# Performance work log

Measured on AMD Instinct MI355X. Metric: run time of the kernel, lower is better.

## Reference

```python
import jax, jax.numpy as jnp
import numpy as np

C_LOGIT = 10.0  # logit range hyperparameter (use_tanh=True)


def setup_inputs() -> dict:
    key = jax.random.key(0)
    ks = jax.random.split(key, 7)
    B, S, D = 64, 2048, 512
    s = 1.0 / np.sqrt(D)
    return {
        "query": jax.random.normal(ks[0], (B, D), jnp.float32),
        "ref": jax.random.normal(ks[1], (B, S, D), jnp.float32),
        "Wq_w": jax.random.uniform(ks[2], (D, D), jnp.float32, -s, s),
        "Wq_b": jax.random.uniform(ks[3], (D,), jnp.float32, -s, s),
        "Wr_w": jax.random.uniform(ks[4], (D, D), jnp.float32, -s, s),  # Conv1d k=1 == Linear
        "Wr_b": jax.random.uniform(ks[5], (D,), jnp.float32, -s, s),
        "value": jax.random.uniform(ks[6], (D,), jnp.float32, -s, s),
    }


def reference(query, ref, Wq_w, Wq_b, Wr_w, Wr_b, value):
    # query: [B, D], ref: [B, S, D]
    q = query @ Wq_w.T + Wq_b                                  # [B, D]  (Wq linear)
    r = jnp.einsum("bsd,ed->bse", ref, Wr_w) + Wr_b            # [B, S, D] (Conv1d k=1 over permuted ref)
    h = jnp.tanh(q[:, None, :] + r)                            # broadcast query over seq_len
    logits = jnp.einsum("bsd,d->bs", h, value)                 # <v, tanh(Wq q + Wr r)>
    logits = C_LOGIT * jnp.tanh(logits)                        # use_tanh=True
    ref_out = jnp.transpose(r, (0, 2, 1))                      # [B, D, S] as returned by torch branch
    return ref_out, logits
```

## Files before the change

### kernel.cpp

```cpp
#include <hip/hip_runtime.h>
#include <stdint.h>

#define NB  64
#define SEQ 2048
#define DIM 512
#define NS  (NB*SEQ)

typedef __bf16 bf16x8 __attribute__((ext_vector_type(8)));
typedef float  f32x4  __attribute__((ext_vector_type(4)));
typedef unsigned int u32;
typedef unsigned short u16;
typedef unsigned int u32x4 __attribute__((ext_vector_type(4)));

__device__ __forceinline__ u32 pk_bf16(float a, float b){
  union {float f; u32 i;} x, y; x.f = a; y.f = b;
  return ((x.i + 0x8000u) >> 16) | ((y.i + 0x8000u) & 0xffff0000u);
}
__device__ __forceinline__ float fast_tanh(float x){
  float e = __builtin_amdgcn_exp2f(x * 2.885390081777927f);
  return 1.0f - 2.0f*__builtin_amdgcn_rcpf(e + 1.0f);
}

__global__ void wconv_kernel(const float* __restrict__ Wr_w, u16* __restrict__ wrbf)
{
  const int i = blockIdx.x*256 + threadIdx.x;
  const int eb = i >> 10, kt = (i >> 6) & 15, quad = (i >> 4) & 3, col = i & 15;
  const float* g = Wr_w + (size_t)(eb*16 + col)*DIM + kt*32 + quad*8;
  f32x4 a = *(const f32x4*)g, c = *(const f32x4*)(g + 4);
  u32x4 p;
  p[0]=pk_bf16(a.x,a.y); p[1]=pk_bf16(a.z,a.w);
  p[2]=pk_bf16(c.x,c.y); p[3]=pk_bf16(c.z,c.w);
  ((u32x4*)wrbf)[i] = p;
}

__global__ void q_kernel(const float* __restrict__ query, const float* __restrict__ Wq_w,
                         const float* __restrict__ Wq_b, float* __restrict__ qws)
{
  __shared__ float lq[DIM];
  const int b   = blockIdx.x;
  const int tid = threadIdx.x;
  const int e   = blockIdx.y*256 + tid;
  for (int i = tid; i < DIM; i += 256) lq[i] = query[b*DIM + i];
  __syncthreads();
  const float* wr = Wq_w + (size_t)e*DIM;
  float acc = 0.f;
  for (int d = 0; d < DIM; d += 4){
    f32x4 w = *(const f32x4*)(wr + d);
    acc += w.x*lq[d] + w.y*lq[d+1] + w.z*lq[d+2] + w.w*lq[d+3];
  }
  qws[b*DIM + e] = acc + Wq_b[e];
}

#define BN 64

__global__ __launch_bounds__(256, 2)
void main_kernel(const float* __restrict__ ref,  const u16* __restrict__ wrbf,
                 const float* __restrict__ Wr_b, const float* __restrict__ value,
                 const float* __restrict__ qws,  float* __restrict__ out)
{
  __shared__ __align__(16) char smem[66560];
  char*  refL = smem;
  float* lred = (float*)(smem + 65536);

  const int tid  = threadIdx.x;
  const int lane = tid & 63, wave = tid >> 6;
  const int col  = lane & 15, quad = lane >> 4;
  const size_t s0 = (size_t)blockIdx.x * BN;
  const int b  = (int)(s0 >> 11);
  const int sb = (int)(s0 & 2047);

#pragma unroll 4
  for (int it = 0; it < 16; ++it){
    const int c   = it*256 + tid;
    const int row = c >> 6, ch = c & 63;
    const float* g = ref + (s0 + row)*DIM + ch*8;
    f32x4 x0 = *(const f32x4*)g, x1 = *(const f32x4*)(g+4);
    u32x4 p;
    p[0]=pk_bf16(x0.x,x0.y); p[1]=pk_bf16(x0.z,x0.w);
    p[2]=pk_bf16(x1.x,x1.y); p[3]=pk_bf16(x1.z,x1.w);
    *(u32x4*)(refL + row*1024 + (ch ^ (row&7))*16) = p;
  }
  __syncthreads();

  f32x4 acc[4][2][4];
#pragma unroll
  for (int et = 0; et < 4; ++et)
#pragma unroll
    for (int mi = 0; mi < 2; ++mi)
#pragma unroll
      for (int ni = 0; ni < 4; ++ni) acc[et][mi][ni] = (f32x4)0.0f;

  auto wptr = [&](int et, int mi, int kt){
    const int eb = et*8 + wave*2 + mi;
    return (const bf16x8*)(wrbf + ((size_t)((eb*16 + kt)*64 + lane))*8);
  };

  bf16x8 wbuf[2][2];
  wbuf[0][0] = *wptr(0, 0, 0);
  wbuf[0][1] = *wptr(0, 1, 0);
  bf16x8 rf[4];

  for (int kt = 0; kt < 16; ++kt){
#pragma unroll
    for (int ni = 0; ni < 4; ++ni){
      const int r = ni*16 + col;
      rf[ni] = *(const bf16x8*)(refL + r*1024 + (((kt*4 + quad) ^ (r&7)))*16);
    }
#pragma unroll
    for (int et = 0; et < 4; ++et){
      const int p = et & 1;
      if (!(kt == 15 && et == 3)){
        const int ne = (et + 1) & 3, nk = (et == 3) ? kt + 1 : kt;
        wbuf[p^1][0] = *wptr(ne, 0, nk);
        wbuf[p^1][1] = *wptr(ne, 1, nk);
      }
#pragma unroll
      for (int mi = 0; mi < 2; ++mi)
#pragma unroll
        for (int ni = 0; ni < 4; ++ni)
          acc[et][mi][ni] = __builtin_amdgcn_mfma_f32_16x16x32_bf16(
                              rf[ni], wbuf[p][mi], acc[et][mi][ni], 0, 0, 0);
    }
  }

  float ls[4][4];
#pragma unroll
  for (int ni = 0; ni < 4; ++ni)
#pragma unroll
    for (int rg = 0; rg < 4; ++rg) ls[ni][rg] = 0.f;

#pragma unroll
  for (int et = 0; et < 4; ++et){
#pragma unroll
    for (int mi = 0; mi < 2; ++mi){
      const int e = et*128 + wave*32 + mi*16 + col;
      const float bb = Wr_b[e];
      const float qq = qws[b*DIM + e];
      const float vv = value[e];
      float* orow = out + ((size_t)(b*DIM + e))*SEQ + sb + quad*4;
#pragma unroll
      for (int ni = 0; ni < 4; ++ni){
        f32x4 v = acc[et][mi][ni];
        v.x += bb; v.y += bb; v.z += bb; v.w += bb;
        *(f32x4*)(orow + ni*16) = v;
        ls[ni][0] += fast_tanh(qq + v.x) * vv;
        ls[ni][1] += fast_tanh(qq + v.y) * vv;
        ls[ni][2] += fast_tanh(qq + v.z) * vv;
        ls[ni][3] += fast_tanh(qq + v.w) * vv;
      }
    }
  }

#pragma unroll
  for (int ni = 0; ni < 4; ++ni)
#pragma unroll
    for (int rg = 0; rg < 4; ++rg){
      float x = ls[ni][rg];
      x += __shfl_xor(x, 1); x += __shfl_xor(x, 2);
      x += __shfl_xor(x, 4); x += __shfl_xor(x, 8);
      ls[ni][rg] = x;
    }
  if (col == 0){
#pragma unroll
    for (int ni = 0; ni < 4; ++ni)
#pragma unroll
      for (int rg = 0; rg < 4; ++rg)
        lred[wave*64 + ni*16 + quad*4 + rg] = ls[ni][rg];
  }
  __syncthreads();
  if (tid < BN){
    const float s = lred[tid] + lred[64+tid] + lred[128+tid] + lred[192+tid];
    out[(size_t)NB*DIM*SEQ + b*SEQ + sb + tid] = 10.0f * fast_tanh(s);
  }
}

extern "C" void kernel_launch(void* const* d_in, const int* in_sizes, int n_in,
                              void* d_out, int out_size, void* d_ws, size_t ws_size,
                              hipStream_t stream)
{
  const float* query = (const float*)d_in[0];
  const float* ref   = (const float*)d_in[1];
  const float* Wq_w  = (const float*)d_in[2];
  const float* Wq_b  = (const float*)d_in[3];
  const float* Wr_w  = (const float*)d_in[4];
  const float* Wr_b  = (const float*)d_in[5];
  const float* value = (const float*)d_in[6];
  float* out = (float*)d_out;

  float* qws  = (float*)d_ws;
  u16*   wrbf = (u16*)((float*)d_ws + NB*DIM);

  wconv_kernel<<<dim3(128), dim3(256), 0, stream>>>(Wr_w, wrbf);
  q_kernel<<<dim3(NB, 2), dim3(256), 0, stream>>>(query, Wq_w, Wq_b, qws);
  main_kernel<<<dim3(NS/BN), dim3(256), 0, stream>>>(ref, wrbf, Wr_b, value, qws, out);
}
```

Before: 534.8 us.

## Split output dim into two halves with deeper weight prefetch and early epilogue

The GEMM over the 512 output features is split into two halves of 256. Each half uses a smaller accumulator array, then writes its results and tanh partial sums before the second half reuses the same registers. Weight fragments are prefetched two K-steps ahead in a 4-deep register ring, and LDS ref fragments are double-buffered one step ahead. Bias, q and value loads are hoisted before the ref staging so their latency is hidden. The aim is to cut register pressure and overlap stores with the second half's MFMA work. The cost is more in-flight weight registers and a fully unrolled 32-step loop, which may enlarge code size.

```diff
diff --git a/kernel.cpp b/kernel.cpp
--- a/kernel.cpp
+++ b/kernel.cpp
@@ -69,6 +69,23 @@
   const int b  = (int)(s0 >> 11);
   const int sb = (int)(s0 & 2047);
 
+  auto wptr = [&](int K, int f){
+    const int eh = K >> 4, kt = K & 15;
+    const int eb = eh*16 + (f>>1)*8 + wave*2 + (f&1);
+    return (const bf16x8*)(wrbf + ((size_t)((eb*16 + kt)*64 + lane))*8);
+  };
+
+  bf16x8 wb[4][4];
+#pragma unroll
+  for (int f = 0; f < 4; ++f) wb[0][f] = *wptr(0, f);
+
+  float bb[8], qq[8], vv[8];
+#pragma unroll
+  for (int i = 0; i < 8; ++i){
+    const int e = (i>>2)*256 + ((i>>1)&1)*128 + wave*32 + (i&1)*16 + col;
+    bb[i] = Wr_b[e]; qq[i] = qws[b*DIM + e]; vv[i] = value[e];
+  }
+
 #pragma unroll 4
   for (int it = 0; it < 16; ++it){
     const int c   = it*256 + tid;
@@ -80,75 +97,74 @@
     p[2]=pk_bf16(x1.x,x1.y); p[3]=pk_bf16(x1.z,x1.w);
     *(u32x4*)(refL + row*1024 + (ch ^ (row&7))*16) = p;
   }
+#pragma unroll
+  for (int f = 0; f < 4; ++f) wb[1][f] = *wptr(1, f);
   __syncthreads();
 
-  f32x4 acc[4][2][4];
-#pragma unroll
-  for (int et = 0; et < 4; ++et)
+  f32x4 acc[2][2][4];
+#pragma unroll
+  for (int et = 0; et < 2; ++et)
 #pragma unroll
     for (int mi = 0; mi < 2; ++mi)
 #pragma unroll
       for (int ni = 0; ni < 4; ++ni) acc[et][mi][ni] = (f32x4)0.0f;
-
-  auto wptr = [&](int et, int mi, int kt){
-    const int eb = et*8 + wave*2 + mi;
-    return (const bf16x8*)(wrbf + ((size_t)((eb*16 + kt)*64 + lane))*8);
-  };
-
-  bf16x8 wbuf[2][2];
-  wbuf[0][0] = *wptr(0, 0, 0);
-  wbuf[0][1] = *wptr(0, 1, 0);
-  bf16x8 rf[4];
-
-  for (int kt = 0; kt < 16; ++kt){
-#pragma unroll
-    for (int ni = 0; ni < 4; ++ni){
-      const int r = ni*16 + col;
-      rf[ni] = *(const bf16x8*)(refL + r*1024 + (((kt*4 + quad) ^ (r&7)))*16);
+  float ls[4][4];
+#pragma unroll
+  for (int ni = 0; ni < 4; ++ni)
+#pragma unroll
+    for (int rg = 0; rg < 4; ++rg) ls[ni][rg] = 0.f;
+
+  bf16x8 rbuf[2][4];
+#pragma unroll
+  for (int ni = 0; ni < 4; ++ni){
+    const int r = ni*16 + col;
+    rbuf[0][ni] = *(const bf16x8*)(refL + r*1024 + ((quad ^ (r&7)))*16);
+  }
+
+#pragma unroll
+  for (int eh = 0; eh < 2; ++eh){
+#pragma unroll
+    for (int kt = 0; kt < 16; ++kt){
+      const int K = eh*16 + kt;
+      if (K + 2 < 32){
+#pragma unroll
+        for (int f = 0; f < 4; ++f) wb[(K+2)&3][f] = *wptr(K+2, f);
+      }
+      if (K + 1 < 32){
+        const int nk = (K+1) & 15;
+#pragma unroll
+        for (int ni = 0; ni < 4; ++ni){
+          const int r = ni*16 + col;
+          rbuf[(K+1)&1][ni] = *(const bf16x8*)(refL + r*1024 + (((nk*4 + quad) ^ (r&7)))*16);
+        }
+      }
+#pragma unroll
+      for (int f = 0; f < 4; ++f)
+#pragma unroll
+        for (int ni = 0; ni < 4; ++ni)
+          acc[f>>1][f&1][ni] = __builtin_amdgcn_mfma_f32_16x16x32_bf16(
+              rbuf[K&1][ni], wb[K&3][f], acc[f>>1][f&1][ni], 0, 0, 0);
     }
-#pragma unroll
-    for (int et = 0; et < 4; ++et){
-      const int p = et & 1;
-      if (!(kt == 15 && et == 3)){
-        const int ne = (et + 1) & 3, nk = (et == 3) ? kt + 1 : kt;
-        wbuf[p^1][0] = *wptr(ne, 0, nk);
-        wbuf[p^1][1] = *wptr(ne, 1, nk);
+
+#pragma unroll
+    for (int et = 0; et < 2; ++et)
+#pragma unroll
+      for (int mi = 0; mi < 2; ++mi){
+        const int i = eh*4 + et*2 + mi;
+        const int e = eh*256 + et*128 + wave*32 + mi*16 + col;
+        float* orow = out + ((size_t)(b*DIM + e))*SEQ + sb + quad*4;
+#pragma unroll
+        for (int ni = 0; ni < 4; ++ni){
+          f32x4 v = acc[et][mi][ni];
+          v.x += bb[i]; v.y += bb[i]; v.z += bb[i]; v.w += bb[i];
+          *(f32x4*)(orow + ni*16) = v;
+          ls[ni][0] += fast_tanh(qq[i] + v.x) * vv[i];
+          ls[ni][1] += fast_tanh(qq[i] + v.y) * vv[i];
+          ls[ni][2] += fast_tanh(qq[i] + v.z) * vv[i];
+          ls[ni][3] += fast_tanh(qq[i] + v.w) * vv[i];
+          if (eh == 0) acc[et][mi][ni] = (f32x4)0.0f;
+        }
       }
-#pragma unroll
-      for (int mi = 0; mi < 2; ++mi)
-#pragma unroll
-        for (int ni = 0; ni < 4; ++ni)
-          acc[et][mi][ni] = __builtin_amdgcn_mfma_f32_16x16x32_bf16(
-                              rf[ni], wbuf[p][mi], acc[et][mi][ni], 0, 0, 0);
-    }
-  }
-
-  float ls[4][4];
-#pragma unroll
-  for (int ni = 0; ni < 4; ++ni)
-#pragma unroll
-    for (int rg = 0; rg < 4; ++rg) ls[ni][rg] = 0.f;
-
-#pragma unroll
-  for (int et = 0; et < 4; ++et){
-#pragma unroll
-    for (int mi = 0; mi < 2; ++mi){
-      const int e = et*128 + wave*32 + mi*16 + col;
-      const float bb = Wr_b[e];
-      const float qq = qws[b*DIM + e];
-      const float vv = value[e];
-      float* orow = out + ((size_t)(b*DIM + e))*SEQ + sb + quad*4;
-#pragma unroll
-      for (int ni = 0; ni < 4; ++ni){
-        f32x4 v = acc[et][mi][ni];
-        v.x += bb; v.y += bb; v.z += bb; v.w += bb;
-        *(f32x4*)(orow + ni*16) = v;
-        ls[ni][0] += fast_tanh(qq + v.x) * vv;
-        ls[ni][1] += fast_tanh(qq + v.y) * vv;
-        ls[ni][2] += fast_tanh(qq + v.z) * vv;
-        ls[ni][3] += fast_tanh(qq + v.w) * vv;
-      }
-    }
   }
 
 #pragma unroll
```

Result: faster. 522.4 us (-2.3%).

## Shrink main kernel tile to 32 rows with 512 threads and deeper prefetch

Applied to the files above, without the earlier changes.

The main GEMM+tanh kernel moves from 64-row tiles with 256 threads to 32-row tiles with 512 threads. Each of 8 waves now owns 64 output features, which cuts the per-thread accumulator count and halves LDS per block. The goal is higher occupancy, more blocks to overlap the memory-bound ref loads and output stores, and hidden latency. It adds 3-stage register prefetch of weights, double-buffered LDS fragment reads, and bias/q/value loads hoisted above the tile load. The trade-off is that each block rereads the full bf16 weight matrix for half as many rows, doubling weight traffic from L2.

```diff
diff --git a/kernel.cpp b/kernel.cpp
--- a/kernel.cpp
+++ b/kernel.cpp
@@ -51,108 +51,109 @@
   qws[b*DIM + e] = acc + Wq_b[e];
 }
 
-#define BN 64
-
-__global__ __launch_bounds__(256, 2)
+__global__ __launch_bounds__(512, 4)
 void main_kernel(const float* __restrict__ ref,  const u16* __restrict__ wrbf,
                  const float* __restrict__ Wr_b, const float* __restrict__ value,
                  const float* __restrict__ qws,  float* __restrict__ out)
 {
-  __shared__ __align__(16) char smem[66560];
-  char*  refL = smem;
-  float* lred = (float*)(smem + 65536);
+  __shared__ __align__(16) char smem[33792];
+  float* lred = (float*)(smem + 32768);
 
   const int tid  = threadIdx.x;
   const int lane = tid & 63, wave = tid >> 6;
   const int col  = lane & 15, quad = lane >> 4;
-  const size_t s0 = (size_t)blockIdx.x * BN;
+  const size_t s0 = (size_t)blockIdx.x * 32;
   const int b  = (int)(s0 >> 11);
   const int sb = (int)(s0 & 2047);
 
-#pragma unroll 4
-  for (int it = 0; it < 16; ++it){
-    const int c   = it*256 + tid;
+  float bb[4], qq[4], vv[4];
+#pragma unroll
+  for (int mi = 0; mi < 4; ++mi){
+    const int e = wave*64 + mi*16 + col;
+    bb[mi] = Wr_b[e]; qq[mi] = qws[b*DIM + e]; vv[mi] = value[e];
+  }
+
+  auto wptr = [&](int kt, int mi){
+    return (const bf16x8*)(wrbf + ((size_t)(((wave*4 + mi)*16 + kt)*64 + lane))*8);
+  };
+
+  bf16x8 wb[3][4];
+#pragma unroll
+  for (int mi = 0; mi < 4; ++mi) wb[0][mi] = *wptr(0, mi);
+#pragma unroll
+  for (int mi = 0; mi < 4; ++mi) wb[1][mi] = *wptr(1, mi);
+
+#pragma unroll
+  for (int it = 0; it < 4; ++it){
+    const int c   = it*512 + tid;
     const int row = c >> 6, ch = c & 63;
     const float* g = ref + (s0 + row)*DIM + ch*8;
     f32x4 x0 = *(const f32x4*)g, x1 = *(const f32x4*)(g+4);
     u32x4 p;
     p[0]=pk_bf16(x0.x,x0.y); p[1]=pk_bf16(x0.z,x0.w);
     p[2]=pk_bf16(x1.x,x1.y); p[3]=pk_bf16(x1.z,x1.w);
-    *(u32x4*)(refL + row*1024 + (ch ^ (row&7))*16) = p;
+    *(u32x4*)(smem + row*1024 + (ch ^ (row&7))*16) = p;
   }
   __syncthreads();
 
-  f32x4 acc[4][2][4];
+  bf16x8 rbuf[2][2];
 #pragma unroll
-  for (int et = 0; et < 4; ++et)
+  for (int ni = 0; ni < 2; ++ni){
+    const int r = ni*16 + col;
+    rbuf[0][ni] = *(const bf16x8*)(smem + r*1024 + ((quad ^ (r&7)))*16);
+  }
+
+  f32x4 acc[4][2];
 #pragma unroll
-    for (int mi = 0; mi < 2; ++mi)
+  for (int mi = 0; mi < 4; ++mi)
 #pragma unroll
-      for (int ni = 0; ni < 4; ++ni) acc[et][mi][ni] = (f32x4)0.0f;
+    for (int ni = 0; ni < 2; ++ni) acc[mi][ni] = (f32x4)0.0f;
 
-  auto wptr = [&](int et, int mi, int kt){
-    const int eb = et*8 + wave*2 + mi;
-    return (const bf16x8*)(wrbf + ((size_t)((eb*16 + kt)*64 + lane))*8);
-  };
-
-  bf16x8 wbuf[2][2];
-  wbuf[0][0] = *wptr(0, 0, 0);
-  wbuf[0][1] = *wptr(0, 1, 0);
-  bf16x8 rf[4];
-
+#pragma unroll
   for (int kt = 0; kt < 16; ++kt){
+    if (kt + 2 < 16){
 #pragma unroll
-    for (int ni = 0; ni < 4; ++ni){
-      const int r = ni*16 + col;
-      rf[ni] = *(const bf16x8*)(refL + r*1024 + (((kt*4 + quad) ^ (r&7)))*16);
+      for (int mi = 0; mi < 4; ++mi) wb[(kt+2)%3][mi] = *wptr(kt+2, mi);
+    }
+    if (kt < 15){
+#pragma unroll
+      for (int ni = 0; ni < 2; ++ni){
+        const int r = ni*16 + col;
+        rbuf[(kt+1)&1][ni] = *(const bf16x8*)(smem + r*1024 + ((((kt+1)*4+quad) ^ (r&7)))*16);
+      }
     }
 #pragma unroll
-    for (int et = 0; et < 4; ++et){
-      const int p = et & 1;
-      if (!(kt == 15 && et == 3)){
-        const int ne = (et + 1) & 3, nk = (et == 3) ? kt + 1 : kt;
-        wbuf[p^1][0] = *wptr(ne, 0, nk);
-        wbuf[p^1][1] = *wptr(ne, 1, nk);
-      }
+    for (int mi = 0; mi < 4; ++mi)
 #pragma unroll
-      for (int mi = 0; mi < 2; ++mi)
-#pragma unroll
-        for (int ni = 0; ni < 4; ++ni)
-          acc[et][mi][ni] = __builtin_amdgcn_mfma_f32_16x16x32_bf16(
-                              rf[ni], wbuf[p][mi], acc[et][mi][ni], 0, 0, 0);
-    }
+      for (int ni = 0; ni < 2; ++ni)
+        acc[mi][ni] = __builtin_amdgcn_mfma_f32_16x16x32_bf16(
+            rbuf[kt&1][ni], wb[kt%3][mi], acc[mi][ni], 0, 0, 0);
   }
 
-  float ls[4][4];
+  float ls[2][4];
 #pragma unroll
-  for (int ni = 0; ni < 4; ++ni)
+  for (int ni = 0; ni < 2; ++ni)
 #pragma unroll
     for (int rg = 0; rg < 4; ++rg) ls[ni][rg] = 0.f;
 
 #pragma unroll
-  for (int et = 0; et < 4; ++et){
+  for (int mi = 0; mi < 4; ++mi){
+    const int e = wave*64 + mi*16 + col;
+    float* orow = out + ((size_t)(b*DIM + e))*SEQ + sb + quad*4;
 #pragma unroll
-    for (int mi = 0; mi < 2; ++mi){
-      const int e = et*128 + wave*32 + mi*16 + col;
-      const float bb = Wr_b[e];
-      const float qq = qws[b*DIM + e];
-      const float vv = value[e];
-      float* orow = out + ((size_t)(b*DIM + e))*SEQ + sb + quad*4;
-#pragma unroll
-      for (int ni = 0; ni < 4; ++ni){
-        f32x4 v = acc[et][mi][ni];
-        v.x += bb; v.y += bb; v.z += bb; v.w += bb;
-        *(f32x4*)(orow + ni*16) = v;
-        ls[ni][0] += fast_tanh(qq + v.x) * vv;
-        ls[ni][1] += fast_tanh(qq + v.y) * vv;
-        ls[ni][2] += fast_tanh(qq + v.z) * vv;
-        ls[ni][3] += fast_tanh(qq + v.w) * vv;
-      }
+    for (int ni = 0; ni < 2; ++ni){
+      f32x4 v = acc[mi][ni];
+      v.x += bb[mi]; v.y += bb[mi]; v.z += bb[mi]; v.w += bb[mi];
+      *(f32x4*)(orow + ni*16) = v;
+      ls[ni][0] += fast_tanh(qq[mi] + v.x) * vv[mi];
+      ls[ni][1] += fast_tanh(qq[mi] + v.y) * vv[mi];
+      ls[ni][2] += fast_tanh(qq[mi] + v.z) * vv[mi];
+      ls[ni][3] += fast_tanh(qq[mi] + v.w) * vv[mi];
     }
   }
 
 #pragma unroll
-  for (int ni = 0; ni < 4; ++ni)
+  for (int ni = 0; ni < 2; ++ni)
 #pragma unroll
     for (int rg = 0; rg < 4; ++rg){
       float x = ls[ni][rg];
@@ -162,15 +163,17 @@
     }
   if (col == 0){
 #pragma unroll
-    for (int ni = 0; ni < 4; ++ni)
+    for (int ni = 0; ni < 2; ++ni)
 #pragma unroll
       for (int rg = 0; rg < 4; ++rg)
-        lred[wave*64 + ni*16 + quad*4 + rg] = ls[ni][rg];
+        lred[wave*32 + ni*16 + quad*4 + rg] = ls[ni][rg];
   }
   __syncthreads();
-  if (tid < BN){
-    const float s = lred[tid] + lred[64+tid] + lred[128+tid] + lred[192+tid];
-    out[(size_t)NB*DIM*SEQ + b*SEQ + sb + tid] = 10.0f * fast_tanh(s);
+  if (tid < 32){
+    float s = 0.f;
+#pragma unroll
+    for (int w = 0; w < 8; ++w) s += lred[w*32 + tid];
+    out[(size_t)NB*DIM*SEQ + (size_t)b*SEQ + sb + tid] = 10.0f * fast_tanh(s);
   }
 }
 
@@ -192,5 +195,5 @@
 
   wconv_kernel<<<dim3(128), dim3(256), 0, stream>>>(Wr_w, wrbf);
   q_kernel<<<dim3(NB, 2), dim3(256), 0, stream>>>(query, Wq_w, Wq_b, qws);
-  main_kernel<<<dim3(NS/BN), dim3(256), 0, stream>>>(ref, wrbf, Wr_b, value, qws, out);
+  main_kernel<<<dim3(NS/32), dim3(512), 0, stream>>>(ref, wrbf, Wr_b, value, qws, out);
 }
```

After: 534.5 us. No clear change (-0.1%).
